# Optimization experiments

Hardware: AMD Instinct MI355X
Metric: run time of the kernel (lower is better)

The kernel has to match this reference:

```python
import jax, jax.numpy as jnp
import numpy as np

MD = 4          # max displacement (pad of 4 on each side; rbot buffers are H+8, W+8)
D = 2 * MD + 1  # 9 displacements per axis -> 81 correlation channels


def setup_inputs() -> dict:
    key = jax.random.key(0)
    k1, k2 = jax.random.split(key)
    B, C, H, W = 4, 128, 192, 192
    tensorFirst = jax.random.normal(k1, (B, D * D, H, W), dtype=jnp.float32)
    tensorSecond = jax.random.normal(k2, (B, C, H, W), dtype=jnp.float32)
    return {"tensorFirst": tensorFirst, "tensorSecond": tensorSecond}


def _corr_transpose(tensorFirst, tensorSecond):
    # out[b,c,y,x] = (1/C) * sum_{p,o in [-4,4]} first[b,(p+4)*9+(o+4),y,x] * second_pad[b,c,y+p,x+o]
    # (zero padding of 4 on each spatial side, matching the rbot rearrange buffers)
    B, C, H, W = tensorSecond.shape
    sec_pad = jnp.pad(tensorSecond, ((0, 0), (0, 0), (MD, MD), (MD, MD)))
    out = jnp.zeros_like(tensorSecond)
    for p in range(-MD, MD + 1):          # fixed 9x9 displacement window
        for o in range(-MD, MD + 1):
            k = (p + MD) * D + (o + MD)
            shifted = sec_pad[:, :, p + MD:p + MD + H, o + MD:o + MD + W]  # [B,C,H,W]
            out = out + tensorFirst[:, k:k + 1] * shifted
    return out / jnp.asarray(C, tensorSecond.dtype)


def reference(tensorFirst, tensorSecond):
    return _corr_transpose(tensorFirst, tensorSecond)
```

## Files before the change

kernel.cpp:

```cpp
#include <hip/hip_runtime.h>

#define MD 4
#define DD 9
#define KK 81
#define B_ 4
#define C_ 128
#define H_ 192
#define W_ 192
#define HW (H_ * W_)
#define NWG 4608
#define PER_XCD (NWG / 8)


__device__ __forceinline__ void unpack12(float (&s)[12],
                                         const float4& A, const float4& M,
                                         const float4& E,
                                         bool edge, bool mA, bool mE) {
  s[0] = A.x; s[1] = A.y; s[2]  = A.z; s[3]  = A.w;
  s[4] = M.x; s[5] = M.y; s[6]  = M.z; s[7]  = M.w;
  s[8] = E.x; s[9] = E.y; s[10] = E.z; s[11] = E.w;
  if (edge) {
    if (!mA) { s[0] = 0.f; s[1] = 0.f; s[2]  = 0.f; s[3]  = 0.f; }
    if (!mE) { s[8] = 0.f; s[9] = 0.f; s[10] = 0.f; s[11] = 0.f; }
  }
}

#define FMA_GROUP(accp, s)                                   \
  _Pragma("unroll")                                          \
  for (int o = 0; o < DD; ++o) {                             \
    accp[0] = fmaf(fo[o].x, s[o + 0], accp[0]);              \
    accp[1] = fmaf(fo[o].y, s[o + 1], accp[1]);              \
    accp[2] = fmaf(fo[o].z, s[o + 2], accp[2]);              \
    accp[3] = fmaf(fo[o].w, s[o + 3], accp[3]);              \
  }

__global__ __launch_bounds__(256, 1)
void corr_transpose_kernel(const float* __restrict__ first,
                           const float* __restrict__ second,
                           float* __restrict__ out) {
  __shared__ __align__(16) float ldsF[KK * 64];

  const int lin = blockIdx.x;
  const int wid = (lin & 7) * PER_XCD + (lin >> 3);
  const int y     = wid % H_;
  const int t     = wid / H_;
  const int chalf = t & 1;
  const int xt0   = ((t >> 1) % 3) * 64;
  const int b     = t / 6;

  const int tid = threadIdx.x;

  {
    const float* fbase = first + ((size_t)(b * KK) * H_ + y) * (size_t)W_ + xt0;
    for (int idx = tid; idx < KK * 16; idx += 256) {
      const int k  = idx >> 4;
      const int xi = (idx & 15) << 2;
      *reinterpret_cast<float4*>(&ldsF[k * 64 + xi]) =
          *reinterpret_cast<const float4*>(fbase + (size_t)k * HW + xi);
    }
  }

  const int xg = tid & 15;
  const int cg = tid >> 4;
  const int c0 = chalf * 64 + cg * 4;
  const int x0 = xt0 + xg * 4;

  const bool mA = (x0 != 0);
  const bool mE = (x0 + 8 <= W_);
  const int  oa = mA ? x0 - 4 : 0;
  const int  oe = mE ? x0 + 4 : W_ - 8;
  const bool edge = (xt0 != 64);

  const int pstart = (y >= MD) ? 0 : (MD - y);
  const int pend   = (y + MD < H_) ? DD : (H_ + MD - y);
  const int yy0    = y + pstart - MD;

  const float* secB = second + (size_t)b * C_ * HW;
  const float* rp0 = secB + ((size_t)c0 * H_ + yy0) * (size_t)W_;
  const float* rp1 = rp0 + HW;
  const float* rp2 = rp1 + HW;
  const float* rp3 = rp2 + HW;

  float4 gA0 = *reinterpret_cast<const float4*>(rp0 + oa);
  float4 gM0 = *reinterpret_cast<const float4*>(rp0 + x0);
  float4 gE0 = *reinterpret_cast<const float4*>(rp0 + oe);
  float4 gA1 = *reinterpret_cast<const float4*>(rp1 + oa);
  float4 gM1 = *reinterpret_cast<const float4*>(rp1 + x0);
  float4 gE1 = *reinterpret_cast<const float4*>(rp1 + oe);

  __syncthreads();

  float acc0[4] = {0.f, 0.f, 0.f, 0.f};
  float acc1[4] = {0.f, 0.f, 0.f, 0.f};
  float acc2[4] = {0.f, 0.f, 0.f, 0.f};
  float acc3[4] = {0.f, 0.f, 0.f, 0.f};

  for (int p = pstart; p < pend; ++p) {
    float4 fo[DD];
#pragma unroll
    for (int o = 0; o < DD; ++o)
      fo[o] = *reinterpret_cast<const float4*>(&ldsF[(p * DD + o) * 64 + (xg << 2)]);

    float4 hA0 = *reinterpret_cast<const float4*>(rp2 + oa);
    float4 hM0 = *reinterpret_cast<const float4*>(rp2 + x0);
    float4 hE0 = *reinterpret_cast<const float4*>(rp2 + oe);
    float4 hA1 = *reinterpret_cast<const float4*>(rp3 + oa);
    float4 hM1 = *reinterpret_cast<const float4*>(rp3 + x0);
    float4 hE1 = *reinterpret_cast<const float4*>(rp3 + oe);

    {
      float s[12];
      unpack12(s, gA0, gM0, gE0, edge, mA, mE);
      FMA_GROUP(acc0, s);
      float u[12];
      unpack12(u, gA1, gM1, gE1, edge, mA, mE);
      FMA_GROUP(acc1, u);
    }

    const int adv = (p + 1 < pend) ? W_ : 0;
    rp0 += adv; rp1 += adv; rp2 += adv; rp3 += adv;

    gA0 = *reinterpret_cast<const float4*>(rp0 + oa);
    gM0 = *reinterpret_cast<const float4*>(rp0 + x0);
    gE0 = *reinterpret_cast<const float4*>(rp0 + oe);
    gA1 = *reinterpret_cast<const float4*>(rp1 + oa);
    gM1 = *reinterpret_cast<const float4*>(rp1 + x0);
    gE1 = *reinterpret_cast<const float4*>(rp1 + oe);

    {
      float s[12];
      unpack12(s, hA0, hM0, hE0, edge, mA, mE);
      FMA_GROUP(acc2, s);
      float u[12];
      unpack12(u, hA1, hM1, hE1, edge, mA, mE);
      FMA_GROUP(acc3, u);
    }
  }

  const float inv_c = 1.0f / (float)C_;
  float* outB = out + (size_t)b * C_ * HW + (size_t)y * W_ + x0;
  {
    float4 v;
    v.x = acc0[0] * inv_c; v.y = acc0[1] * inv_c;
    v.z = acc0[2] * inv_c; v.w = acc0[3] * inv_c;
    *reinterpret_cast<float4*>(outB + (size_t)(c0 + 0) * HW) = v;
    v.x = acc1[0] * inv_c; v.y = acc1[1] * inv_c;
    v.z = acc1[2] * inv_c; v.w = acc1[3] * inv_c;
    *reinterpret_cast<float4*>(outB + (size_t)(c0 + 1) * HW) = v;
    v.x = acc2[0] * inv_c; v.y = acc2[1] * inv_c;
    v.z = acc2[2] * inv_c; v.w = acc2[3] * inv_c;
    *reinterpret_cast<float4*>(outB + (size_t)(c0 + 2) * HW) = v;
    v.x = acc3[0] * inv_c; v.y = acc3[1] * inv_c;
    v.z = acc3[2] * inv_c; v.w = acc3[3] * inv_c;
    *reinterpret_cast<float4*>(outB + (size_t)(c0 + 3) * HW) = v;
  }
}

extern "C" void kernel_launch(void* const* d_in, const int* in_sizes, int n_in,
                              void* d_out, int out_size, void* d_ws, size_t ws_size,
                              hipStream_t stream) {
  const float* first  = (const float*)d_in[0];
  const float* second = (const float*)d_in[1];
  float* out = (float*)d_out;

  corr_transpose_kernel<<<dim3(NWG), 256, 0, stream>>>(first, second, out);
}
```

Before: 90.57 us.

## Load first-tensor weights directly from global instead of LDS staging

Removes the LDS staging of the 81-channel first-tensor tile and the block barrier, so each thread reads its nine float4 weights per displacement row straight from global memory (relying on cache reuse across the 16 channel-group threads). The software-pipelined prefetch of second-tensor rows is replaced by issuing all twelve loads at the top of each iteration, and launch bounds drop the one-block-per-CU minimum. This removes LDS traffic, the staging prologue and the sync, but multiplies global/L1 requests for the first tensor and loses explicit load/compute overlap.

```diff
diff --git a/kernel.cpp b/kernel.cpp
--- a/kernel.cpp
+++ b/kernel.cpp
@@ -34,12 +34,10 @@
     accp[3] = fmaf(fo[o].w, s[o + 3], accp[3]);              \
   }
 
-__global__ __launch_bounds__(256, 1)
+__global__ __launch_bounds__(256)
 void corr_transpose_kernel(const float* __restrict__ first,
                            const float* __restrict__ second,
                            float* __restrict__ out) {
-  __shared__ __align__(16) float ldsF[KK * 64];
-
   const int lin = blockIdx.x;
   const int wid = (lin & 7) * PER_XCD + (lin >> 3);
   const int y     = wid % H_;
@@ -49,17 +47,6 @@
   const int b     = t / 6;
 
   const int tid = threadIdx.x;
-
-  {
-    const float* fbase = first + ((size_t)(b * KK) * H_ + y) * (size_t)W_ + xt0;
-    for (int idx = tid; idx < KK * 16; idx += 256) {
-      const int k  = idx >> 4;
-      const int xi = (idx & 15) << 2;
-      *reinterpret_cast<float4*>(&ldsF[k * 64 + xi]) =
-          *reinterpret_cast<const float4*>(fbase + (size_t)k * HW + xi);
-    }
-  }
-
   const int xg = tid & 15;
   const int cg = tid >> 4;
   const int c0 = chalf * 64 + cg * 4;
@@ -75,20 +62,14 @@
   const int pend   = (y + MD < H_) ? DD : (H_ + MD - y);
   const int yy0    = y + pstart - MD;
 
+  const float* fp =
+      first + ((size_t)(b * KK + pstart * DD) * H_ + y) * (size_t)W_ + x0;
+
   const float* secB = second + (size_t)b * C_ * HW;
   const float* rp0 = secB + ((size_t)c0 * H_ + yy0) * (size_t)W_;
   const float* rp1 = rp0 + HW;
   const float* rp2 = rp1 + HW;
   const float* rp3 = rp2 + HW;
-
-  float4 gA0 = *reinterpret_cast<const float4*>(rp0 + oa);
-  float4 gM0 = *reinterpret_cast<const float4*>(rp0 + x0);
-  float4 gE0 = *reinterpret_cast<const float4*>(rp0 + oe);
-  float4 gA1 = *reinterpret_cast<const float4*>(rp1 + oa);
-  float4 gM1 = *reinterpret_cast<const float4*>(rp1 + x0);
-  float4 gE1 = *reinterpret_cast<const float4*>(rp1 + oe);
-
-  __syncthreads();
 
   float acc0[4] = {0.f, 0.f, 0.f, 0.f};
   float acc1[4] = {0.f, 0.f, 0.f, 0.f};
@@ -98,43 +79,46 @@
   for (int p = pstart; p < pend; ++p) {
     float4 fo[DD];
 #pragma unroll
-    for (int o = 0; o < DD; ++o)
-      fo[o] = *reinterpret_cast<const float4*>(&ldsF[(p * DD + o) * 64 + (xg << 2)]);
+    for (int o = 0; o < DD; ++o) {
+      fo[o] = *reinterpret_cast<const float4*>(fp);
+      fp += HW;
+    }
 
-    float4 hA0 = *reinterpret_cast<const float4*>(rp2 + oa);
-    float4 hM0 = *reinterpret_cast<const float4*>(rp2 + x0);
-    float4 hE0 = *reinterpret_cast<const float4*>(rp2 + oe);
-    float4 hA1 = *reinterpret_cast<const float4*>(rp3 + oa);
-    float4 hM1 = *reinterpret_cast<const float4*>(rp3 + x0);
-    float4 hE1 = *reinterpret_cast<const float4*>(rp3 + oe);
+    float4 A0 = *reinterpret_cast<const float4*>(rp0 + oa);
+    float4 M0 = *reinterpret_cast<const float4*>(rp0 + x0);
+    float4 E0 = *reinterpret_cast<const float4*>(rp0 + oe);
+    float4 A1 = *reinterpret_cast<const float4*>(rp1 + oa);
+    float4 M1 = *reinterpret_cast<const float4*>(rp1 + x0);
+    float4 E1 = *reinterpret_cast<const float4*>(rp1 + oe);
+    float4 A2 = *reinterpret_cast<const float4*>(rp2 + oa);
+    float4 M2 = *reinterpret_cast<const float4*>(rp2 + x0);
+    float4 E2 = *reinterpret_cast<const float4*>(rp2 + oe);
+    float4 A3 = *reinterpret_cast<const float4*>(rp3 + oa);
+    float4 M3 = *reinterpret_cast<const float4*>(rp3 + x0);
+    float4 E3 = *reinterpret_cast<const float4*>(rp3 + oe);
 
     {
       float s[12];
-      unpack12(s, gA0, gM0, gE0, edge, mA, mE);
+      unpack12(s, A0, M0, E0, edge, mA, mE);
       FMA_GROUP(acc0, s);
-      float u[12];
-      unpack12(u, gA1, gM1, gE1, edge, mA, mE);
-      FMA_GROUP(acc1, u);
+    }
+    {
+      float s[12];
+      unpack12(s, A1, M1, E1, edge, mA, mE);
+      FMA_GROUP(acc1, s);
+    }
+    {
+      float s[12];
+      unpack12(s, A2, M2, E2, edge, mA, mE);
+      FMA_GROUP(acc2, s);
+    }
+    {
+      float s[12];
+      unpack12(s, A3, M3, E3, edge, mA, mE);
+      FMA_GROUP(acc3, s);
     }
 
-    const int adv = (p + 1 < pend) ? W_ : 0;
-    rp0 += adv; rp1 += adv; rp2 += adv; rp3 += adv;
-
-    gA0 = *reinterpret_cast<const float4*>(rp0 + oa);
-    gM0 = *reinterpret_cast<const float4*>(rp0 + x0);
-    gE0 = *reinterpret_cast<const float4*>(rp0 + oe);
-    gA1 = *reinterpret_cast<const float4*>(rp1 + oa);
-    gM1 = *reinterpret_cast<const float4*>(rp1 + x0);
-    gE1 = *reinterpret_cast<const float4*>(rp1 + oe);
-
-    {
-      float s[12];
-      unpack12(s, hA0, hM0, hE0, edge, mA, mE);
-      FMA_GROUP(acc2, s);
-      float u[12];
-      unpack12(u, hA1, hM1, hE1, edge, mA, mE);
-      FMA_GROUP(acc3, u);
-    }
+    rp0 += W_; rp1 += W_; rp2 += W_; rp3 += W_;
   }
 
   const float inv_c = 1.0f / (float)C_;
```

New measurement: 107.7 us. 18.9% more time.
